# Kernel optimization log

Hardware: AMD Instinct MI355X
Metric: run time of the kernel (lower is better)

The kernel has to match this reference:

```python
import jax, jax.numpy as jnp
import numpy as np

B, T, D, H, L = 32, 512, 1024, 1024, 2


def setup_inputs() -> dict:
    key = jax.random.key(0)
    ks = jax.random.split(key, 8)
    s_in = 1.0 / np.sqrt(D)   # approximate orthogonal-init scale
    s_h = 1.0 / np.sqrt(H)
    return {
        "x": jax.random.normal(ks[0], (B, T, D), jnp.float32),
        "hidden": jnp.zeros((L, B, H), jnp.float32),
        "w_ih0": jax.random.normal(ks[1], (3 * H, D), jnp.float32) * s_in,
        "w_hh0": jax.random.normal(ks[2], (3 * H, H), jnp.float32) * s_h,
        "b_ih0": jnp.zeros((3 * H,), jnp.float32),
        "b_hh0": jnp.zeros((3 * H,), jnp.float32),
        "w_ih1": jax.random.normal(ks[3], (3 * H, H), jnp.float32) * s_h,
        "w_hh1": jax.random.normal(ks[4], (3 * H, H), jnp.float32) * s_h,
        "b_ih1": jnp.zeros((3 * H,), jnp.float32),
        "b_hh1": jnp.zeros((3 * H,), jnp.float32),
    }


def _gru_layer(x, h0, w_ih, w_hh, b_ih, b_hh):
    # x: [B,T,Din] -> precompute input projection once (as in source)
    xp = jnp.einsum('btd,gd->btg', x, w_ih) + b_ih        # [B,T,3H]
    xp_t = jnp.swapaxes(xp, 0, 1)                          # [T,B,3H]

    def step(h, xpt):
        hp = h @ w_hh.T + b_hh                             # [B,3H]
        r = jax.nn.sigmoid(xpt[:, :H] + hp[:, :H])
        z = jax.nn.sigmoid(xpt[:, H:2 * H] + hp[:, H:2 * H])
        n = jnp.tanh(xpt[:, 2 * H:] + r * hp[:, 2 * H:])
        h_new = (1 - z) * n + z * h
        return h_new, h_new

    h_last, ys = jax.lax.scan(step, h0, xp_t)              # ys: [T,B,H]
    return jnp.swapaxes(ys, 0, 1), h_last


def reference(x, hidden, w_ih0, w_hh0, b_ih0, b_hh0,
              w_ih1, w_hh1, b_ih1, b_hh1):
    y0, h0 = _gru_layer(x, hidden[0], w_ih0, w_hh0, b_ih0, b_hh0)
    y1, h1 = _gru_layer(y0, hidden[1], w_ih1, w_hh1, b_ih1, b_hh1)
    # dropout rates are 0.0 (eval semantics) -> identity
    return y1, jnp.stack([h0, h1], axis=0)
```

## Files before the change

### kernel.cpp

```cpp
#include <hip/hip_runtime.h>
#include <hip/hip_bf16.h>

#define NB 32
#define NT 512
#define NH 1024
#define G3 3072
#define NWG 128
#define LDS_BLOB 98304
#define LDS_PART 16384
#define LDS_HPF  8192
#define LDS_HLOC 2048
#define PK_LDS (LDS_BLOB + LDS_PART + LDS_HPF + LDS_HLOC)

typedef __attribute__((ext_vector_type(8))) short short8;
typedef __attribute__((ext_vector_type(4))) float f32x4;
typedef __attribute__((ext_vector_type(4))) unsigned short us4;
typedef unsigned long long u64;

static __device__ __forceinline__ unsigned short f2bf(float f) {
    union { float f; unsigned u; } v; v.f = f;
    if ((v.u & 0x7fffffffu) > 0x7f800000u) return (unsigned short)((v.u >> 16) | 0x0040u);
    unsigned u = v.u + 0x7fffu + ((v.u >> 16) & 1u);
    return (unsigned short)(u >> 16);
}

static __device__ __forceinline__ void coh_store8(u64* p, u64 v) {
    __hip_atomic_store(p, v, __ATOMIC_RELAXED, __HIP_MEMORY_SCOPE_AGENT);
}

static __device__ __forceinline__ void coh_load_1KB(const char* base, short8 o[16]) {
    asm volatile(
        "global_load_dwordx4 %0,  %16, off sc0 sc1\n\t"
        "global_load_dwordx4 %1,  %16, off offset:64 sc0 sc1\n\t"
        "global_load_dwordx4 %2,  %16, off offset:128 sc0 sc1\n\t"
        "global_load_dwordx4 %3,  %16, off offset:192 sc0 sc1\n\t"
        "global_load_dwordx4 %4,  %16, off offset:256 sc0 sc1\n\t"
        "global_load_dwordx4 %5,  %16, off offset:320 sc0 sc1\n\t"
        "global_load_dwordx4 %6,  %16, off offset:384 sc0 sc1\n\t"
        "global_load_dwordx4 %7,  %16, off offset:448 sc0 sc1\n\t"
        "global_load_dwordx4 %8,  %16, off offset:512 sc0 sc1\n\t"
        "global_load_dwordx4 %9,  %16, off offset:576 sc0 sc1\n\t"
        "global_load_dwordx4 %10, %16, off offset:640 sc0 sc1\n\t"
        "global_load_dwordx4 %11, %16, off offset:704 sc0 sc1\n\t"
        "global_load_dwordx4 %12, %16, off offset:768 sc0 sc1\n\t"
        "global_load_dwordx4 %13, %16, off offset:832 sc0 sc1\n\t"
        "global_load_dwordx4 %14, %16, off offset:896 sc0 sc1\n\t"
        "global_load_dwordx4 %15, %16, off offset:960 sc0 sc1\n\t"
        "s_waitcnt vmcnt(0)"
        : "=&v"(o[0]), "=&v"(o[1]), "=&v"(o[2]), "=&v"(o[3]),
          "=&v"(o[4]), "=&v"(o[5]), "=&v"(o[6]), "=&v"(o[7]),
          "=&v"(o[8]), "=&v"(o[9]), "=&v"(o[10]), "=&v"(o[11]),
          "=&v"(o[12]), "=&v"(o[13]), "=&v"(o[14]), "=&v"(o[15])
        : "v"(base)
        : "memory");
    __builtin_amdgcn_sched_barrier(0);
}

__global__ __launch_bounds__(256) void cvt_bf16_v4(const float4* __restrict__ src,
                                                   us4* __restrict__ dst, int n4) {
    for (int i = blockIdx.x * 256 + threadIdx.x; i < n4; i += gridDim.x * 256) {
        float4 v = src[i];
        us4 o;
        o.x = f2bf(v.x); o.y = f2bf(v.y); o.z = f2bf(v.z); o.w = f2bf(v.w);
        dst[i] = o;
    }
}

__global__ __launch_bounds__(256) void txp_x(const float4* __restrict__ x, us4* __restrict__ xt) {
    const int total = NT * NB * 256;
    for (int i = blockIdx.x * 256 + threadIdx.x; i < total; i += gridDim.x * 256) {
        int b = i / (NT * 256);
        int rem = i - b * (NT * 256);
        int t = rem >> 8;
        int d4 = rem & 255;
        float4 v = x[i];
        us4 o;
        o.x = f2bf(v.x); o.y = f2bf(v.y); o.z = f2bf(v.z); o.w = f2bf(v.w);
        xt[((size_t)t * NB + b) * 256 + d4] = o;
    }
}

__global__ __launch_bounds__(256) void init_h(const float* __restrict__ hid,
                                              unsigned short* __restrict__ h0b,
                                              unsigned short* __restrict__ h1b) {
    int i = blockIdx.x * 256 + threadIdx.x;
    h0b[i] = f2bf(hid[i]);
    h1b[i] = f2bf(hid[NB * NH + i]);
}

__global__ __launch_bounds__(256, 1) void gru_persistent(
    const unsigned short* __restrict__ xt,
    unsigned short* __restrict__ y0b,
    const unsigned short* __restrict__ wih0, const unsigned short* __restrict__ whh0,
    const unsigned short* __restrict__ wih1, const unsigned short* __restrict__ whh1,
    const float* __restrict__ bih0, const float* __restrict__ bhh0,
    const float* __restrict__ bih1, const float* __restrict__ bhh1,
    const float* __restrict__ hid,
    unsigned short* __restrict__ hb00, unsigned short* __restrict__ hb01,
    unsigned short* __restrict__ hb10, unsigned short* __restrict__ hb11,
    float* __restrict__ out,
    int* __restrict__ flags)
{
    extern __shared__ char lds[];
    short* blob = (short*)lds;
    float* part = (float*)(lds + LDS_BLOB);
    float* hpf  = (float*)(lds + LDS_BLOB + LDS_PART);
    float* hloc = (float*)(lds + LDS_BLOB + LDS_PART + LDS_HPF);

    const int tid  = threadIdx.x;
    const int lane = tid & 63;
    const int wv   = tid >> 6;
    const int kh   = wv & 1;
    const int mt   = wv >> 1;
    const int lr   = lane & 15;
    const int lq   = lane >> 4;

    const int wg   = blockIdx.x;
    const int lay  = wg >> 6;
    const int slot = wg & 63;
    const int j0   = slot * 16;

    const int* poll_own = flags + lay * 128 + mt * 64 + lane;
    const int* poll_y0  = flags + mt * 64 + lane;
    int* pub = flags + lay * 128 + (tid >> 6) * 64 + slot;

    const unsigned short* wih = lay ? wih1 : wih0;
    const unsigned short* whh = lay ? whh1 : whh0;
    const float* bih = lay ? bih1 : bih0;
    const float* bhh = lay ? bhh1 : bhh0;
    unsigned short* hb[2];
    if (lay == 0) { hb[0] = hb00; hb[1] = hb01; }
    else          { hb[0] = hb10; hb[1] = hb11; }

    for (int c = tid; c < 6144; c += 256) {
        int g   = c >> 11;
        int rem = c & 2047;
        int kt  = rem >> 6;
        int q   = (rem >> 4) & 3;
        int col = rem & 15;
        *(short8*)(blob + c * 8) =
            *(const short8*)((const short*)whh + (size_t)(g * 1024 + j0 + col) * 1024 + kt * 32 + q * 8);
    }

    float br_[4], bz_[4], bxn_[4], bhn_[4];
    if (tid < 128) {
        const int b = tid >> 2, c4 = (tid & 3) * 4;
#pragma unroll
        for (int j = 0; j < 4; ++j) {
            int gc = j0 + c4 + j;
            br_[j]  = bih[gc] + bhh[gc];
            bz_[j]  = bih[1024 + gc] + bhh[1024 + gc];
            bxn_[j] = bih[2048 + gc];
            bhn_[j] = bhh[2048 + gc];
        }
        float4 h0 = *(const float4*)&hid[(size_t)lay * NB * NH + (size_t)b * 1024 + j0 + c4];
        *(float4*)&hloc[b * 16 + c4] = h0;
    }
    __syncthreads();

    const int aoff = (mt * 16 + lr) * 1024 + lq * 8;
    const size_t aoff_b = (size_t)aoff * 2 + (size_t)kh * 1024;
    const short* wiB = (const short*)wih + (size_t)(j0 + lr) * 1024 + lq * 8;

    for (int t = 0; t < NT; ++t) {
        f32x4 acc0 = {0.f,0.f,0.f,0.f};
        f32x4 acc1 = {0.f,0.f,0.f,0.f};
        f32x4 acc2 = {0.f,0.f,0.f,0.f};
        f32x4 acc3 = {0.f,0.f,0.f,0.f};

        if (lay == 0) {
            const short* Ap = (const short*)xt + (size_t)t * NB * 1024 + aoff;
#pragma unroll 8
            for (int kk = 0; kk < 16; ++kk) {
                const int kt = kh * 16 + kk;
                short8 a  = *(const short8*)(Ap + kt * 32);
                short8 b0 = *(const short8*)(wiB + kt * 32);
                short8 b1 = *(const short8*)(wiB + 1024 * 1024 + kt * 32);
                short8 b2 = *(const short8*)(wiB + 2 * 1024 * 1024 + kt * 32);
                acc0 = __builtin_amdgcn_mfma_f32_16x16x32_bf16(a, b0, acc0, 0, 0, 0);
                acc1 = __builtin_amdgcn_mfma_f32_16x16x32_bf16(a, b1, acc1, 0, 0, 0);
                acc2 = __builtin_amdgcn_mfma_f32_16x16x32_bf16(a, b2, acc2, 0, 0, 0);
            }
        } else {
            while (__hip_atomic_load(poll_y0, __ATOMIC_RELAXED, __HIP_MEMORY_SCOPE_AGENT) < t + 1)
                __builtin_amdgcn_s_sleep(1);
            asm volatile("" ::: "memory");
            short8 ya[16];
            coh_load_1KB((const char*)y0b + (size_t)t * NB * 1024 * 2 + aoff_b, ya);
#pragma unroll
            for (int kk = 0; kk < 16; ++kk) {
                const int kt = kh * 16 + kk;
                short8 b0 = *(const short8*)(wiB + kt * 32);
                short8 b1 = *(const short8*)(wiB + 1024 * 1024 + kt * 32);
                short8 b2 = *(const short8*)(wiB + 2 * 1024 * 1024 + kt * 32);
                acc0 = __builtin_amdgcn_mfma_f32_16x16x32_bf16(ya[kk], b0, acc0, 0, 0, 0);
                acc1 = __builtin_amdgcn_mfma_f32_16x16x32_bf16(ya[kk], b1, acc1, 0, 0, 0);
                acc2 = __builtin_amdgcn_mfma_f32_16x16x32_bf16(ya[kk], b2, acc2, 0, 0, 0);
            }
        }

        while (__hip_atomic_load(poll_own, __ATOMIC_RELAXED, __HIP_MEMORY_SCOPE_AGENT) < t)
            __builtin_amdgcn_s_sleep(1);
        asm volatile("" ::: "memory");

        {
            short8 ha[16];
            coh_load_1KB((const char*)hb[t & 1] + aoff_b, ha);
#pragma unroll
            for (int kk = 0; kk < 16; ++kk) {
                const int kt = kh * 16 + kk;
                short8 c0 = *(const short8*)(blob + kt * 512 + lane * 8);
                short8 c1 = *(const short8*)(blob + (32 + kt) * 512 + lane * 8);
                short8 c2 = *(const short8*)(blob + (64 + kt) * 512 + lane * 8);
                acc0 = __builtin_amdgcn_mfma_f32_16x16x32_bf16(ha[kk], c0, acc0, 0, 0, 0);
                acc1 = __builtin_amdgcn_mfma_f32_16x16x32_bf16(ha[kk], c1, acc1, 0, 0, 0);
                acc3 = __builtin_amdgcn_mfma_f32_16x16x32_bf16(ha[kk], c2, acc3, 0, 0, 0);
            }
        }

        *(f32x4*)(part + ((wv * 4 + 0) * 64 + lane) * 4) = acc0;
        *(f32x4*)(part + ((wv * 4 + 1) * 64 + lane) * 4) = acc1;
        *(f32x4*)(part + ((wv * 4 + 2) * 64 + lane) * 4) = acc2;
        *(f32x4*)(part + ((wv * 4 + 3) * 64 + lane) * 4) = acc3;
        __syncthreads();

        for (int eo = tid; eo < 2048; eo += 256) {
            int g2 = eo >> 9, b = (eo >> 4) & 31, c = eo & 15;
            int m = b >> 4, r = b & 3, l = ((b >> 2) & 3) * 16 + c;
            float v = part[(((m * 2 + 0) * 4 + g2) * 64 + l) * 4 + r]
                    + part[(((m * 2 + 1) * 4 + g2) * 64 + l) * 4 + r];
            hpf[eo] = v;
        }
        __syncthreads();

        if (tid < 128) {
            const int b = tid >> 2, c4 = (tid & 3) * 4;
            const int gc0 = j0 + c4;
            float hn[4];
            u64 hpack = 0;
#pragma unroll
            for (int j = 0; j < 4; ++j) {
                const int e = b * 16 + c4 + j;
                float pr  = hpf[e];
                float pz  = hpf[512 + e];
                float pxn = hpf[1024 + e];
                float phn = hpf[1536 + e];
                float r = 1.f / (1.f + __expf(-(pr + br_[j])));
                float z = 1.f / (1.f + __expf(-(pz + bz_[j])));
                float na = pxn + bxn_[j] + r * (phn + bhn_[j]);
                float e2 = __expf(-2.f * na);
                float n = (1.f - e2) / (1.f + e2);
                float hprev = hloc[e];
                float h = (1.f - z) * n + z * hprev;
                hloc[e] = h;
                hn[j] = h;
                hpack |= (u64)f2bf(h) << (16 * j);
            }
            coh_store8((u64*)((unsigned short*)hb[(t + 1) & 1] + (size_t)b * 1024 + gc0), hpack);
            if (lay == 0)
                coh_store8((u64*)(y0b + ((size_t)t * NB + b) * 1024 + gc0), hpack);

            asm volatile("s_waitcnt vmcnt(0)" ::: "memory");
            if ((tid & 63) == 0)
                __hip_atomic_store(pub, t + 1, __ATOMIC_RELAXED, __HIP_MEMORY_SCOPE_AGENT);

            if (lay == 1) {
                float4 o4; o4.x = hn[0]; o4.y = hn[1]; o4.z = hn[2]; o4.w = hn[3];
                *(float4*)&out[((size_t)b * NT + t) * 1024 + gc0] = o4;
            }
            if (t == NT - 1) {
                float4 o4; o4.x = hn[0]; o4.y = hn[1]; o4.z = hn[2]; o4.w = hn[3];
                *(float4*)&out[(size_t)NB * NT * 1024 + (size_t)lay * NB * NH + (size_t)b * 1024 + gc0] = o4;
            }
        }
    }
}

extern "C" void kernel_launch(void* const* d_in, const int* in_sizes, int n_in,
                              void* d_out, int out_size, void* d_ws, size_t ws_size,
                              hipStream_t stream) {
    (void)in_sizes; (void)n_in; (void)out_size; (void)ws_size;

    const float* x     = (const float*)d_in[0];
    const float* hid   = (const float*)d_in[1];
    const float* w_ih0 = (const float*)d_in[2];
    const float* w_hh0 = (const float*)d_in[3];
    const float* b_ih0 = (const float*)d_in[4];
    const float* b_hh0 = (const float*)d_in[5];
    const float* w_ih1 = (const float*)d_in[6];
    const float* w_hh1 = (const float*)d_in[7];
    const float* b_ih1 = (const float*)d_in[8];
    const float* b_hh1 = (const float*)d_in[9];
    float* out = (float*)d_out;

    char* ws = (char*)d_ws;
    size_t off = 0;
    auto alloc = [&](size_t bytes) -> void* {
        void* p = ws + off;
        off += (bytes + 255) & ~(size_t)255;
        return p;
    };

    unsigned short* xtb   = (unsigned short*)alloc((size_t)NT * NB * 1024 * 2);
    unsigned short* y0b   = (unsigned short*)alloc((size_t)NT * NB * 1024 * 2);
    unsigned short* wih0b = (unsigned short*)alloc((size_t)G3 * 1024 * 2);
    unsigned short* whh0b = (unsigned short*)alloc((size_t)G3 * 1024 * 2);
    unsigned short* wih1b = (unsigned short*)alloc((size_t)G3 * 1024 * 2);
    unsigned short* whh1b = (unsigned short*)alloc((size_t)G3 * 1024 * 2);
    unsigned short* hb0[2]; unsigned short* hb1[2];
    for (int i = 0; i < 2; i++) hb0[i] = (unsigned short*)alloc(NB * NH * 2);
    for (int i = 0; i < 2; i++) hb1[i] = (unsigned short*)alloc(NB * NH * 2);
    int* flags = (int*)alloc(2 * 2 * 64 * sizeof(int));

    txp_x<<<2048, 256, 0, stream>>>((const float4*)x, (us4*)xtb);
    cvt_bf16_v4<<<512, 256, 0, stream>>>((const float4*)w_ih0, (us4*)wih0b, G3 * 1024 / 4);
    cvt_bf16_v4<<<512, 256, 0, stream>>>((const float4*)w_hh0, (us4*)whh0b, G3 * 1024 / 4);
    cvt_bf16_v4<<<512, 256, 0, stream>>>((const float4*)w_ih1, (us4*)wih1b, G3 * 1024 / 4);
    cvt_bf16_v4<<<512, 256, 0, stream>>>((const float4*)w_hh1, (us4*)whh1b, G3 * 1024 / 4);
    init_h<<<NB * NH / 256, 256, 0, stream>>>(hid, hb0[0], hb1[0]);
    hipMemsetAsync(flags, 0, 2 * 2 * 64 * sizeof(int), stream);

    (void)hipFuncSetAttribute((const void*)gru_persistent,
                              hipFuncAttributeMaxDynamicSharedMemorySize, PK_LDS);
    gru_persistent<<<NWG, 256, PK_LDS, stream>>>(
        xtb, y0b, wih0b, whh0b, wih1b, whh1b,
        b_ih0, b_hh0, b_ih1, b_hh1, hid,
        hb0[0], hb0[1], hb1[0], hb1[1],
        out, flags);
}
```

Before: 7.020 ms.

## Prefetch recurrent state before input GEMM and drop a barrier via double-buffered partials

```diff
diff --git a/kernel.cpp b/kernel.cpp
--- a/kernel.cpp
+++ b/kernel.cpp
@@ -7,10 +7,9 @@
 #define G3 3072
 #define NWG 128
 #define LDS_BLOB 98304
-#define LDS_PART 16384
-#define LDS_HPF  8192
+#define LDS_PART 32768
 #define LDS_HLOC 2048
-#define PK_LDS (LDS_BLOB + LDS_PART + LDS_HPF + LDS_HLOC)
+#define PK_LDS (LDS_BLOB + LDS_PART + LDS_HLOC)
 
 typedef __attribute__((ext_vector_type(8))) short short8;
 typedef __attribute__((ext_vector_type(4))) float f32x4;
@@ -28,7 +27,7 @@
     __hip_atomic_store(p, v, __ATOMIC_RELAXED, __HIP_MEMORY_SCOPE_AGENT);
 }
 
-static __device__ __forceinline__ void coh_load_1KB(const char* base, short8 o[16]) {
+static __device__ __forceinline__ void coh_issue16(const char* base, short8 o[16]) {
     asm volatile(
         "global_load_dwordx4 %0,  %16, off sc0 sc1\n\t"
         "global_load_dwordx4 %1,  %16, off offset:64 sc0 sc1\n\t"
@@ -45,16 +44,22 @@
         "global_load_dwordx4 %12, %16, off offset:768 sc0 sc1\n\t"
         "global_load_dwordx4 %13, %16, off offset:832 sc0 sc1\n\t"
         "global_load_dwordx4 %14, %16, off offset:896 sc0 sc1\n\t"
-        "global_load_dwordx4 %15, %16, off offset:960 sc0 sc1\n\t"
-        "s_waitcnt vmcnt(0)"
+        "global_load_dwordx4 %15, %16, off offset:960 sc0 sc1"
         : "=&v"(o[0]), "=&v"(o[1]), "=&v"(o[2]), "=&v"(o[3]),
           "=&v"(o[4]), "=&v"(o[5]), "=&v"(o[6]), "=&v"(o[7]),
           "=&v"(o[8]), "=&v"(o[9]), "=&v"(o[10]), "=&v"(o[11]),
           "=&v"(o[12]), "=&v"(o[13]), "=&v"(o[14]), "=&v"(o[15])
         : "v"(base)
         : "memory");
-    __builtin_amdgcn_sched_barrier(0);
-}
+}
+
+#define VMWAIT_BIND(NSTR, o)                                                   \
+    asm volatile("s_waitcnt vmcnt(" NSTR ")"                                   \
+        : "+v"(o[0]), "+v"(o[1]), "+v"(o[2]), "+v"(o[3]),                      \
+          "+v"(o[4]), "+v"(o[5]), "+v"(o[6]), "+v"(o[7]),                      \
+          "+v"(o[8]), "+v"(o[9]), "+v"(o[10]), "+v"(o[11]),                    \
+          "+v"(o[12]), "+v"(o[13]), "+v"(o[14]), "+v"(o[15]) :: "memory");     \
+    __builtin_amdgcn_sched_barrier(0)
 
 __global__ __launch_bounds__(256) void cvt_bf16_v4(const float4* __restrict__ src,
                                                    us4* __restrict__ dst, int n4) {
@@ -104,8 +109,7 @@
     extern __shared__ char lds[];
     short* blob = (short*)lds;
     float* part = (float*)(lds + LDS_BLOB);
-    float* hpf  = (float*)(lds + LDS_BLOB + LDS_PART);
-    float* hloc = (float*)(lds + LDS_BLOB + LDS_PART + LDS_HPF);
+    float* hloc = (float*)(lds + LDS_BLOB + LDS_PART);
 
     const int tid  = threadIdx.x;
     const int lane = tid & 63;
@@ -167,8 +171,14 @@
         f32x4 acc1 = {0.f,0.f,0.f,0.f};
         f32x4 acc2 = {0.f,0.f,0.f,0.f};
         f32x4 acc3 = {0.f,0.f,0.f,0.f};
+        short8 ha[16];
 
         if (lay == 0) {
+            while (__hip_atomic_load(poll_own, __ATOMIC_RELAXED, __HIP_MEMORY_SCOPE_AGENT) < t)
+                __builtin_amdgcn_s_sleep(4);
+            asm volatile("" ::: "memory");
+            coh_issue16((const char*)hb[t & 1] + aoff_b, ha);
+
             const short* Ap = (const short*)xt + (size_t)t * NB * 1024 + aoff;
 #pragma unroll 8
             for (int kk = 0; kk < 16; ++kk) {
@@ -181,13 +191,20 @@
                 acc1 = __builtin_amdgcn_mfma_f32_16x16x32_bf16(a, b1, acc1, 0, 0, 0);
                 acc2 = __builtin_amdgcn_mfma_f32_16x16x32_bf16(a, b2, acc2, 0, 0, 0);
             }
+            VMWAIT_BIND("0", ha);
         } else {
-            while (__hip_atomic_load(poll_y0, __ATOMIC_RELAXED, __HIP_MEMORY_SCOPE_AGENT) < t + 1)
-                __builtin_amdgcn_s_sleep(1);
+            while (true) {
+                int a  = __hip_atomic_load(poll_y0,  __ATOMIC_RELAXED, __HIP_MEMORY_SCOPE_AGENT);
+                int b2 = __hip_atomic_load(poll_own, __ATOMIC_RELAXED, __HIP_MEMORY_SCOPE_AGENT);
+                if (a >= t + 1 && b2 >= t) break;
+                __builtin_amdgcn_s_sleep(4);
+            }
             asm volatile("" ::: "memory");
             short8 ya[16];
-            coh_load_1KB((const char*)y0b + (size_t)t * NB * 1024 * 2 + aoff_b, ya);
-#pragma unroll
+            coh_issue16((const char*)y0b + (size_t)t * NB * 1024 * 2 + aoff_b, ya);
+            coh_issue16((const char*)hb[t & 1] + aoff_b, ha);
+            VMWAIT_BIND("16", ya);
+#pragma unroll 8
             for (int kk = 0; kk < 16; ++kk) {
                 const int kt = kh * 16 + kk;
                 short8 b0 = *(const short8*)(wiB + kt * 32);
@@ -197,62 +214,51 @@
                 acc1 = __builtin_amdgcn_mfma_f32_16x16x32_bf16(ya[kk], b1, acc1, 0, 0, 0);
                 acc2 = __builtin_amdgcn_mfma_f32_16x16x32_bf16(ya[kk], b2, acc2, 0, 0, 0);
             }
+            VMWAIT_BIND("0", ha);
         }
 
-        while (__hip_atomic_load(poll_own, __ATOMIC_RELAXED, __HIP_MEMORY_SCOPE_AGENT) < t)
-            __builtin_amdgcn_s_sleep(1);
-        asm volatile("" ::: "memory");
-
-        {
-            short8 ha[16];
-            coh_load_1KB((const char*)hb[t & 1] + aoff_b, ha);
-#pragma unroll
-            for (int kk = 0; kk < 16; ++kk) {
-                const int kt = kh * 16 + kk;
-                short8 c0 = *(const short8*)(blob + kt * 512 + lane * 8);
-                short8 c1 = *(const short8*)(blob + (32 + kt) * 512 + lane * 8);
-                short8 c2 = *(const short8*)(blob + (64 + kt) * 512 + lane * 8);
-                acc0 = __builtin_amdgcn_mfma_f32_16x16x32_bf16(ha[kk], c0, acc0, 0, 0, 0);
-                acc1 = __builtin_amdgcn_mfma_f32_16x16x32_bf16(ha[kk], c1, acc1, 0, 0, 0);
-                acc3 = __builtin_amdgcn_mfma_f32_16x16x32_bf16(ha[kk], c2, acc3, 0, 0, 0);
-            }
+#pragma unroll 8
+        for (int kk = 0; kk < 16; ++kk) {
+            const int kt = kh * 16 + kk;
+            short8 c0 = *(const short8*)(blob + kt * 512 + lane * 8);
+            short8 c1 = *(const short8*)(blob + (32 + kt) * 512 + lane * 8);
+            short8 c2 = *(const short8*)(blob + (64 + kt) * 512 + lane * 8);
+            acc0 = __builtin_amdgcn_mfma_f32_16x16x32_bf16(ha[kk], c0, acc0, 0, 0, 0);
+            acc1 = __builtin_amdgcn_mfma_f32_16x16x32_bf16(ha[kk], c1, acc1, 0, 0, 0);
+            acc3 = __builtin_amdgcn_mfma_f32_16x16x32_bf16(ha[kk], c2, acc3, 0, 0, 0);
         }
 
-        *(f32x4*)(part + ((wv * 4 + 0) * 64 + lane) * 4) = acc0;
-        *(f32x4*)(part + ((wv * 4 + 1) * 64 + lane) * 4) = acc1;
-        *(f32x4*)(part + ((wv * 4 + 2) * 64 + lane) * 4) = acc2;
-        *(f32x4*)(part + ((wv * 4 + 3) * 64 + lane) * 4) = acc3;
-        __syncthreads();
-
-        for (int eo = tid; eo < 2048; eo += 256) {
-            int g2 = eo >> 9, b = (eo >> 4) & 31, c = eo & 15;
-            int m = b >> 4, r = b & 3, l = ((b >> 2) & 3) * 16 + c;
-            float v = part[(((m * 2 + 0) * 4 + g2) * 64 + l) * 4 + r]
-                    + part[(((m * 2 + 1) * 4 + g2) * 64 + l) * 4 + r];
-            hpf[eo] = v;
-        }
+        float* pt = part + (t & 1) * 4096;
+        *(f32x4*)(pt + ((wv * 4 + 0) * 64 + lane) * 4) = acc0;
+        *(f32x4*)(pt + ((wv * 4 + 1) * 64 + lane) * 4) = acc1;
+        *(f32x4*)(pt + ((wv * 4 + 2) * 64 + lane) * 4) = acc2;
+        *(f32x4*)(pt + ((wv * 4 + 3) * 64 + lane) * 4) = acc3;
         __syncthreads();
 
         if (tid < 128) {
             const int b = tid >> 2, c4 = (tid & 3) * 4;
             const int gc0 = j0 + c4;
+            const int m = b >> 4, rg = b & 3, lq2 = (b >> 2) & 3;
             float hn[4];
             u64 hpack = 0;
 #pragma unroll
             for (int j = 0; j < 4; ++j) {
-                const int e = b * 16 + c4 + j;
-                float pr  = hpf[e];
-                float pz  = hpf[512 + e];
-                float pxn = hpf[1024 + e];
-                float phn = hpf[1536 + e];
+                const int c = c4 + j;
+                const int l = lq2 * 16 + c;
+                const int i0 = ((m * 2 + 0) * 4) * 64 + l;
+                const int i1 = ((m * 2 + 1) * 4) * 64 + l;
+                float pr  = pt[(i0 + 0 * 64) * 4 + rg] + pt[(i1 + 0 * 64) * 4 + rg];
+                float pz  = pt[(i0 + 1 * 64) * 4 + rg] + pt[(i1 + 1 * 64) * 4 + rg];
+                float pxn = pt[(i0 + 2 * 64) * 4 + rg] + pt[(i1 + 2 * 64) * 4 + rg];
+                float phn = pt[(i0 + 3 * 64) * 4 + rg] + pt[(i1 + 3 * 64) * 4 + rg];
                 float r = 1.f / (1.f + __expf(-(pr + br_[j])));
                 float z = 1.f / (1.f + __expf(-(pz + bz_[j])));
                 float na = pxn + bxn_[j] + r * (phn + bhn_[j]);
                 float e2 = __expf(-2.f * na);
                 float n = (1.f - e2) / (1.f + e2);
-                float hprev = hloc[e];
+                float hprev = hloc[b * 16 + c];
                 float h = (1.f - z) * n + z * hprev;
-                hloc[e] = h;
+                hloc[b * 16 + c] = h;
                 hn[j] = h;
                 hpack |= (u64)f2bf(h) << (16 * j);
             }
```

Result: slower. 11.24 ms (+60.1%).
